# Performance work log

Hardware: AMD Instinct MI355X
Metric: run time of the kernel (lower is better)

The kernel has to match this reference:

```python
import jax, jax.numpy as jnp
import numpy as np

B, V, C, D, H, W = 1, 3, 16, 32, 256, 320


def setup_inputs() -> dict:
    key = jax.random.key(0)
    k1, k2 = jax.random.split(key)
    features = jax.random.normal(k1, (V, B, C, H, W), jnp.float32)
    # intrinsics (4x4 with 3x3 K in top-left), extrinsics with small per-view translation
    K = np.eye(4, dtype=np.float32)
    K[0, 0] = 320.0; K[1, 1] = 320.0; K[0, 2] = W / 2.0; K[1, 2] = H / 2.0
    proj = np.zeros((B, V, 2, 4, 4), np.float32)
    for v in range(V):
        E = np.eye(4, dtype=np.float32)
        E[0, 3] = 0.1 * v; E[1, 3] = 0.05 * v
        proj[:, v, 0] = E
        proj[:, v, 1] = K
    depth = jnp.linspace(425.0, 935.0, D, dtype=jnp.float32)  # DTU-style range
    depth_values = jnp.broadcast_to(depth[None, :, None, None], (B, D, H, W))
    w_reg = jax.random.normal(k2, (C,), jnp.float32) * 0.1
    return dict(features=features, proj_matrices=jnp.asarray(proj),
                depth_values=depth_values, w_reg=w_reg)


def _make_proj(pm):
    # pm: [B,2,4,4]; new[:, :3, :4] = K[:3,:3] @ E[:3,:4]
    top = jnp.einsum('bij,bjk->bik', pm[:, 1, :3, :3], pm[:, 0, :3, :4])
    return pm[:, 0].at[:, :3, :4].set(top)


def _gather_bilinear_corner(flat, xi, yi):
    # flat: [B,C,H*W]; xi, yi: int [B,D,HW] -> [B,C,D,HW] with zero padding
    valid = (xi >= 0) & (xi < W) & (yi >= 0) & (yi < H)
    idx = jnp.clip(yi, 0, H - 1) * W + jnp.clip(xi, 0, W - 1)
    b, d, n = idx.shape
    g = jnp.take_along_axis(flat, idx.reshape(b, 1, d * n), axis=2)
    g = g.reshape(b, flat.shape[1], d, n)
    return g * valid[:, None].astype(flat.dtype)


def homo_warp(src_fea, src_proj, ref_proj, depth_values):
    # src_fea [B,C,H,W], projs [B,4,4], depth_values [B,D,H,W] -> [B,C,D,H,W]
    proj = jnp.einsum('bij,bjk->bik', src_proj, jnp.linalg.inv(ref_proj))
    rot, trans = proj[:, :3, :3], proj[:, :3, 3]
    yy, xx = jnp.meshgrid(jnp.arange(H, dtype=jnp.float32),
                          jnp.arange(W, dtype=jnp.float32), indexing='ij')
    xyz = jnp.stack([xx.ravel(), yy.ravel(), jnp.ones(H * W, jnp.float32)], 0)  # [3,HW]
    rot_xyz = jnp.einsum('bij,jn->bin', rot, xyz)  # [B,3,HW]
    # [B,3,D,HW]
    pxyz = rot_xyz[:, :, None, :] * depth_values.reshape(B, 1, D, H * W) \
           + trans[:, :, None, None]
    z = pxyz[:, 2]
    z = jnp.where(jnp.abs(z) < 1e-6, 1e-6, z)
    px = pxyz[:, 0] / z  # [B,D,HW] pixel x
    py = pxyz[:, 1] / z
    x0 = jnp.floor(px); y0 = jnp.floor(py)
    wx = px - x0; wy = py - y0
    x0i = x0.astype(jnp.int32); y0i = y0.astype(jnp.int32)
    flat = src_fea.reshape(B, C, H * W)
    g00 = _gather_bilinear_corner(flat, x0i, y0i)
    g01 = _gather_bilinear_corner(flat, x0i + 1, y0i)
    g10 = _gather_bilinear_corner(flat, x0i, y0i + 1)
    g11 = _gather_bilinear_corner(flat, x0i + 1, y0i + 1)
    wx = wx[:, None]; wy = wy[:, None]
    out = (g00 * (1 - wx) * (1 - wy) + g01 * wx * (1 - wy)
           + g10 * (1 - wx) * wy + g11 * wx * wy)
    return out.reshape(B, C, D, H, W)


def _forward(features, proj_matrices, depth_values, w_reg):
    ref_fea = features[0]
    ref_proj_new = _make_proj(proj_matrices[:, 0])
    ref_vol = jnp.broadcast_to(ref_fea[:, :, None], (B, C, D, H, W))
    volume_sum = ref_vol
    volume_sq_sum = ref_vol ** 2
    for v in range(1, V):  # small fixed view loop
        src_proj_new = _make_proj(proj_matrices[:, v])
        warped = homo_warp(features[v], src_proj_new, ref_proj_new, depth_values)
        volume_sum = volume_sum + warped
        volume_sq_sum = volume_sq_sum + warped ** 2
    variance = volume_sq_sum / V - (volume_sum / V) ** 2  # [B,C,D,H,W]
    cost = jnp.einsum('bcdhw,c->bdhw', variance, w_reg)
    prob = jax.nn.softmax(cost, axis=1)  # [B,D,H,W]
    depth = jnp.sum(prob * depth_values, axis=1)  # [B,H,W]
    # confidence (no-grad branch): 2*avg_pool3d(kernel (2,1,1)) == adjacent-pair sum
    p = jax.lax.stop_gradient(prob)
    psum = p + jnp.concatenate([p[:, 1:], jnp.zeros_like(p[:, :1])], axis=1)
    didx = jnp.sum(p * jnp.arange(D, dtype=p.dtype)[None, :, None, None], axis=1)
    didx = jnp.clip(didx.astype(jnp.int32), 0, D - 1)
    conf = jnp.take_along_axis(psum, didx[:, None], axis=1)[:, 0]
    return depth, conf, prob


def reference(features, proj_matrices, depth_values, w_reg):
    return _forward(features, proj_matrices, depth_values, w_reg)
```

## Files before the change

kernel.cpp:

```cpp
#include <hip/hip_runtime.h>
#include <math.h>

namespace {
constexpr int NV = 3;
constexpr int NC = 16;
constexpr int ND = 32;
constexpr int NH = 256;
constexpr int NW = 320;
constexpr int HW = NH * NW;
#define SYM(i, j) ((i) * 4 + (j) - (i) * ((i) + 1) / 2)
}

__device__ __forceinline__ float frcp(float z) {
    float r = __builtin_amdgcn_rcpf(z);
    return r * fmaf(-z, r, 2.0f);
}

__global__ __launch_bounds__(256) void mega3_kernel(
    const float* __restrict__ feats,
    const float* __restrict__ pm,
    const float* __restrict__ dvals,
    const float* __restrict__ wreg,
    float* __restrict__ out)
{
    const unsigned tid = blockIdx.x * 256u + threadIdx.x;
    const unsigned n = tid >> 2;
    const int q = (int)(tid & 3u);
    const int d0 = q * 8;
    const int y = (int)(n / NW);
    const int x = (int)(n - (unsigned)y * NW);
    const float fx = (float)x, fy = (float)y;
    const unsigned voff = n * 4u;

    const char* fb = (const char*)feats;
    const char* f1b = fb + (size_t)1 * NC * HW * 4;
    const char* f2b = fb + (size_t)2 * NC * HW * 4;

    const float dep0 = *(const float*)((const char*)dvals + voff);
    float rf[4];
#pragma unroll
    for (int c4 = 0; c4 < 4; ++c4)
        rf[c4] = *(const float*)(fb + (size_t)(q * 4 + c4) * HW * 4 + voff);
    float dv[8];
#pragma unroll
    for (int i = 0; i < 8; ++i)
        dv[i] = *(const float*)((const char*)dvals +
                                (size_t)(d0 + i) * HW * 4 + voff);

    float P[NV][4][4];
#pragma unroll
    for (int v = 0; v < NV; ++v) {
        const float* E = pm + v * 2 * 16;
        const float* K = pm + v * 2 * 16 + 16;
#pragma unroll
        for (int j = 0; j < 4; ++j) P[v][3][j] = E[12 + j];
#pragma unroll
        for (int i = 0; i < 3; ++i)
#pragma unroll
            for (int j = 0; j < 4; ++j) {
                float acc = 0.f;
#pragma unroll
                for (int k = 0; k < 3; ++k) acc += K[i * 4 + k] * E[k * 4 + j];
                P[v][i][j] = acc;
            }
    }
    float Inv[4][4];
    {
        const float m00 = P[0][0][0], m01 = P[0][0][1], m02 = P[0][0][2], m03 = P[0][0][3];
        const float m10 = P[0][1][0], m11 = P[0][1][1], m12 = P[0][1][2], m13 = P[0][1][3];
        const float m20 = P[0][2][0], m21 = P[0][2][1], m22 = P[0][2][2], m23 = P[0][2][3];
        const float m30 = P[0][3][0], m31 = P[0][3][1], m32 = P[0][3][2], m33 = P[0][3][3];
        const float s0 = m00 * m11 - m10 * m01;
        const float s1 = m00 * m12 - m10 * m02;
        const float s2 = m00 * m13 - m10 * m03;
        const float s3 = m01 * m12 - m11 * m02;
        const float s4 = m01 * m13 - m11 * m03;
        const float s5 = m02 * m13 - m12 * m03;
        const float c5 = m22 * m33 - m32 * m23;
        const float c4_ = m21 * m33 - m31 * m23;
        const float c3 = m21 * m32 - m31 * m22;
        const float c2 = m20 * m33 - m30 * m23;
        const float c1 = m20 * m32 - m30 * m22;
        const float c0 = m20 * m31 - m30 * m21;
        const float det = s0 * c5 - s1 * c4_ + s2 * c3 + s3 * c2 - s4 * c1 + s5 * c0;
        const float id = 1.f / det;
        Inv[0][0] = ( m11 * c5 - m12 * c4_ + m13 * c3) * id;
        Inv[0][1] = (-m01 * c5 + m02 * c4_ - m03 * c3) * id;
        Inv[0][2] = ( m31 * s5 - m32 * s4 + m33 * s3) * id;
        Inv[0][3] = (-m21 * s5 + m22 * s4 - m23 * s3) * id;
        Inv[1][0] = (-m10 * c5 + m12 * c2 - m13 * c1) * id;
        Inv[1][1] = ( m00 * c5 - m02 * c2 + m03 * c1) * id;
        Inv[1][2] = (-m30 * s5 + m32 * s2 - m33 * s1) * id;
        Inv[1][3] = ( m20 * s5 - m22 * s2 + m23 * s1) * id;
        Inv[2][0] = ( m10 * c4_ - m11 * c2 + m13 * c0) * id;
        Inv[2][1] = (-m00 * c4_ + m01 * c2 - m03 * c0) * id;
        Inv[2][2] = ( m30 * s4 - m31 * s2 + m33 * s0) * id;
        Inv[2][3] = (-m20 * s4 + m21 * s2 - m23 * s0) * id;
        Inv[3][0] = (-m10 * c3 + m11 * c1 - m12 * c0) * id;
        Inv[3][1] = ( m00 * c3 - m01 * c1 + m02 * c0) * id;
        Inv[3][2] = (-m30 * s3 + m31 * s1 - m32 * s0) * id;
        Inv[3][3] = ( m20 * s3 - m21 * s1 + m22 * s0) * id;
    }
    float rxv[2], ryv[2], rzv[2], t0v[2], t1v[2], t2v[2];
#pragma unroll
    for (int v = 0; v < 2; ++v) {
        float M[3][4];
#pragma unroll
        for (int i = 0; i < 3; ++i)
#pragma unroll
            for (int j = 0; j < 4; ++j) {
                float acc = 0.f;
#pragma unroll
                for (int k = 0; k < 4; ++k) acc += P[v + 1][i][k] * Inv[k][j];
                M[i][j] = acc;
            }
        rxv[v] = fmaf(M[0][0], fx, fmaf(M[0][1], fy, M[0][2]));
        ryv[v] = fmaf(M[1][0], fx, fmaf(M[1][1], fy, M[1][2]));
        rzv[v] = fmaf(M[2][0], fx, fmaf(M[2][1], fy, M[2][2]));
        t0v[v] = M[0][3]; t1v[v] = M[1][3]; t2v[v] = M[2][3];
    }

    int x0r[2], y0r[2];
    unsigned co[2][4];
    float mk[2][4];
#pragma unroll
    for (int v = 0; v < 2; ++v) {
        float pxn = fmaf(rxv[v], dep0, t0v[v]);
        float pyn = fmaf(ryv[v], dep0, t1v[v]);
        float z   = fmaf(rzv[v], dep0, t2v[v]);
        z = (fabsf(z) < 1e-6f) ? 1e-6f : z;
        float ri = frcp(z);
        float px = pxn * ri, py = pyn * ri;
        int x0 = (int)floorf(px), y0 = (int)floorf(py);
        x0r[v] = x0; y0r[v] = y0;
        bool vx0 = (x0 >= 0) && (x0 < NW);
        bool vx1 = (x0 + 1 >= 0) && (x0 + 1 < NW);
        bool vy0 = (y0 >= 0) && (y0 < NH);
        bool vy1 = (y0 + 1 >= 0) && (y0 + 1 < NH);
        mk[v][0] = (vx0 && vy0) ? 1.f : 0.f;
        mk[v][1] = (vx1 && vy0) ? 1.f : 0.f;
        mk[v][2] = (vx0 && vy1) ? 1.f : 0.f;
        mk[v][3] = (vx1 && vy1) ? 1.f : 0.f;
        int cx0 = min(max(x0, 0), NW - 1);
        int cx1 = min(max(x0 + 1, 0), NW - 1);
        int cy0 = min(max(y0, 0), NH - 1);
        int cy1 = min(max(y0 + 1, 0), NH - 1);
        co[v][0] = (unsigned)(cy0 * NW + cx0) * 4u;
        co[v][1] = (unsigned)(cy0 * NW + cx1) * 4u;
        co[v][2] = (unsigned)(cy1 * NW + cx0) * 4u;
        co[v][3] = (unsigned)(cy1 * NW + cx1) * 4u;
    }

    float G1[10], G2[10], Cm[16], R1[4], R2[4];
    float r2 = 0.f;
#pragma unroll
    for (int k = 0; k < 10; ++k) { G1[k] = 0.f; G2[k] = 0.f; }
#pragma unroll
    for (int k = 0; k < 16; ++k) Cm[k] = 0.f;
#pragma unroll
    for (int k = 0; k < 4; ++k) { R1[k] = 0.f; R2[k] = 0.f; }

#pragma unroll
    for (int c4 = 0; c4 < 4; ++c4) {
        const int c = q * 4 + c4;
        const char* f1c = f1b + (size_t)c * HW * 4;
        const char* f2c = f2b + (size_t)c * HW * 4;
        float r = rf[c4];
        float g1[4], g2[4];
#pragma unroll
        for (int i = 0; i < 4; ++i) {
            g1[i] = *(const float*)(f1c + co[0][i]) * mk[0][i];
            g2[i] = *(const float*)(f2c + co[1][i]) * mk[1][i];
        }
        float w = wreg[c];
        float wr = w * r;
        r2 = fmaf(wr, r, r2);
        float wg1[4], wg2[4];
#pragma unroll
        for (int i = 0; i < 4; ++i) { wg1[i] = w * g1[i]; wg2[i] = w * g2[i]; }
#pragma unroll
        for (int i = 0; i < 4; ++i) {
            R1[i] = fmaf(wr, g1[i], R1[i]);
            R2[i] = fmaf(wr, g2[i], R2[i]);
        }
#pragma unroll
        for (int i = 0; i < 4; ++i)
#pragma unroll
            for (int j = i; j < 4; ++j) {
                G1[SYM(i, j)] = fmaf(wg1[i], g1[j], G1[SYM(i, j)]);
                G2[SYM(i, j)] = fmaf(wg2[i], g2[j], G2[SYM(i, j)]);
            }
#pragma unroll
        for (int i = 0; i < 4; ++i)
#pragma unroll
            for (int j = 0; j < 4; ++j)
                Cm[i * 4 + j] = fmaf(wg1[i], g2[j], Cm[i * 4 + j]);
    }

#pragma unroll
    for (int k = 0; k < 10; ++k) {
        G1[k] += __shfl_xor(G1[k], 1); G1[k] += __shfl_xor(G1[k], 2);
        G2[k] += __shfl_xor(G2[k], 1); G2[k] += __shfl_xor(G2[k], 2);
    }
#pragma unroll
    for (int k = 0; k < 16; ++k) {
        Cm[k] += __shfl_xor(Cm[k], 1); Cm[k] += __shfl_xor(Cm[k], 2);
    }
#pragma unroll
    for (int k = 0; k < 4; ++k) {
        R1[k] += __shfl_xor(R1[k], 1); R1[k] += __shfl_xor(R1[k], 2);
        R2[k] += __shfl_xor(R2[k], 1); R2[k] += __shfl_xor(R2[k], 2);
    }
    r2 += __shfl_xor(r2, 1); r2 += __shfl_xor(r2, 2);

    static constexpr float U2[3][3] = {{1.f,-2.f,1.f},{0.f,1.f,-1.f},{0.f,0.f,1.f}};
    static constexpr float U1[2][2] = {{1.f,-1.f},{0.f,1.f}};
    float A[9], Bp[9], Xc[16];
#pragma unroll
    for (int k = 0; k < 9; ++k) { A[k] = 0.f; Bp[k] = 0.f; }
#pragma unroll
    for (int k = 0; k < 16; ++k) Xc[k] = 0.f;
    A[0] = r2;
#pragma unroll
    for (int i = 0; i < 4; ++i) {
#pragma unroll
        for (int j = 0; j < 4; ++j) {
            const int lo = i < j ? i : j, hi = i < j ? j : i;
            const float g1v = G1[SYM(lo, hi)];
            const float g2v = G2[SYM(lo, hi)];
            const int m = i & 1, kk = i >> 1, nn = j & 1, ll = j >> 1;
#pragma unroll
            for (int p = 0; p < 3; ++p)
#pragma unroll
                for (int qq = 0; qq < 3; ++qq) {
                    const float cc = U2[m + nn][p] * U2[kk + ll][qq];
                    if (cc != 0.f) {
                        A[p * 3 + qq] += g1v * cc;
                        Bp[p * 3 + qq] += g2v * cc;
                    }
                }
        }
    }
#pragma unroll
    for (int i = 0; i < 4; ++i) {
        const int m = i & 1, kk = i >> 1;
#pragma unroll
        for (int p = 0; p < 2; ++p)
#pragma unroll
            for (int qq = 0; qq < 2; ++qq) {
                const float cc = U1[m][p] * U1[kk][qq];
                if (cc != 0.f) {
                    A[p * 3 + qq] -= R1[i] * cc;
                    Bp[p * 3 + qq] -= R2[i] * cc;
                }
            }
    }
#pragma unroll
    for (int i = 0; i < 4; ++i) {
        const int m = i & 1, kk = i >> 1;
#pragma unroll
        for (int j = 0; j < 4; ++j) {
            const int nn = j & 1, ll = j >> 1;
            const float cv = Cm[i * 4 + j];
#pragma unroll
            for (int p = 0; p < 2; ++p)
#pragma unroll
                for (int qq = 0; qq < 2; ++qq)
#pragma unroll
                    for (int rr = 0; rr < 2; ++rr)
#pragma unroll
                        for (int ss = 0; ss < 2; ++ss) {
                            const float cc = U1[m][p] * U1[kk][qq]
                                           * U1[nn][rr] * U1[ll][ss];
                            if (cc != 0.f)
                                Xc[p * 8 + qq * 4 + rr * 2 + ss] -= cv * cc;
                        }
        }
    }

    float c[8];
    float mx = -INFINITY;
#pragma unroll
    for (int ck = 0; ck < 2; ++ck) {
        float pxs[2][4], pys[2][4];
#pragma unroll
        for (int dd = 0; dd < 4; ++dd) {
            const float depth = dv[ck * 4 + dd];
#pragma unroll
            for (int v = 0; v < 2; ++v) {
                float pxn = fmaf(rxv[v], depth, t0v[v]);
                float pyn = fmaf(ryv[v], depth, t1v[v]);
                float z   = fmaf(rzv[v], depth, t2v[v]);
                z = (fabsf(z) < 1e-6f) ? 1e-6f : z;
                float ri = frcp(z);
                pxs[v][dd] = pxn * ri;
                pys[v][dd] = pyn * ri;
            }
        }
#pragma unroll
        for (int dd = 0; dd < 4; ++dd) {
            float wx[2], wy[2];
            int ax0[2], ay0[2];
            bool fast = true;
#pragma unroll
            for (int v = 0; v < 2; ++v) {
                float px = pxs[v][dd], py = pys[v][dd];
                float x0f = floorf(px), y0f = floorf(py);
                wx[v] = px - x0f;
                wy[v] = py - y0f;
                int x0 = (int)x0f, y0 = (int)y0f;
                ax0[v] = x0; ay0[v] = y0;
                fast = fast && (x0 == x0r[v]) && (y0 == y0r[v]);
            }

            float cst;
            if (fast) {
                const float wx0 = wx[0], wy0 = wy[0];
                const float wx1 = wx[1], wy1 = wy[1];
                float a0 = fmaf(wy0, fmaf(wy0, A[2], A[1]), A[0]);
                float a1 = fmaf(wy0, fmaf(wy0, A[5], A[4]), A[3]);
                float a2 = fmaf(wy0, fmaf(wy0, A[8], A[7]), A[6]);
                float PA = fmaf(wx0, fmaf(wx0, a2, a1), a0);
                float b0 = fmaf(wy1, fmaf(wy1, Bp[2], Bp[1]), Bp[0]);
                float b1 = fmaf(wy1, fmaf(wy1, Bp[5], Bp[4]), Bp[3]);
                float b2 = fmaf(wy1, fmaf(wy1, Bp[8], Bp[7]), Bp[6]);
                float PB = fmaf(wx1, fmaf(wx1, b2, b1), b0);
                float y0_ = fmaf(wy1, Xc[1], Xc[0]);
                float y1_ = fmaf(wy1, Xc[3], Xc[2]);
                float y2_ = fmaf(wy1, Xc[5], Xc[4]);
                float y3_ = fmaf(wy1, Xc[7], Xc[6]);
                float y4_ = fmaf(wy1, Xc[9], Xc[8]);
                float y5_ = fmaf(wy1, Xc[11], Xc[10]);
                float y6_ = fmaf(wy1, Xc[13], Xc[12]);
                float y7_ = fmaf(wy1, Xc[15], Xc[14]);
                float z0_ = fmaf(wx1, y1_, y0_);
                float z1_ = fmaf(wx1, y3_, y2_);
                float z2_ = fmaf(wx1, y5_, y4_);
                float z3_ = fmaf(wx1, y7_, y6_);
                float w0_ = fmaf(wy0, z1_, z0_);
                float w1_ = fmaf(wy0, z3_, z2_);
                float Xv = fmaf(wx0, w1_, w0_);
                cst = (2.f / 9.f) * (PA + PB + Xv);
            } else {
                float al[2][4];
                unsigned so[2][4];
#pragma unroll
                for (int v = 0; v < 2; ++v) {
                    int x0 = ax0[v], y0 = ay0[v];
                    bool vx0 = (x0 >= 0) && (x0 < NW);
                    bool vx1 = (x0 + 1 >= 0) && (x0 + 1 < NW);
                    bool vy0 = (y0 >= 0) && (y0 < NH);
                    bool vy1 = (y0 + 1 >= 0) && (y0 + 1 < NH);
                    float wxx = wx[v], wyy = wy[v];
                    al[v][0] = (1.f - wxx) * (1.f - wyy) * ((vx0 && vy0) ? 1.f : 0.f);
                    al[v][1] = wxx * (1.f - wyy) * ((vx1 && vy0) ? 1.f : 0.f);
                    al[v][2] = (1.f - wxx) * wyy * ((vx0 && vy1) ? 1.f : 0.f);
                    al[v][3] = wxx * wyy * ((vx1 && vy1) ? 1.f : 0.f);
                    int cx0 = min(max(x0, 0), NW - 1);
                    int cx1 = min(max(x0 + 1, 0), NW - 1);
                    int cy0 = min(max(y0, 0), NH - 1);
                    int cy1 = min(max(y0 + 1, 0), NH - 1);
                    so[v][0] = (unsigned)(cy0 * NW + cx0) * 4u;
                    so[v][1] = (unsigned)(cy0 * NW + cx1) * 4u;
                    so[v][2] = (unsigned)(cy1 * NW + cx0) * 4u;
                    so[v][3] = (unsigned)(cy1 * NW + cx1) * 4u;
                }
                float acc = 0.f;
#pragma unroll
                for (int cc = 0; cc < NC; ++cc) {
                    const char* frc = fb + (size_t)cc * HW * 4;
                    const char* f1c = f1b + (size_t)cc * HW * 4;
                    const char* f2c = f2b + (size_t)cc * HW * 4;
                    float r = *(const float*)(frc + voff);
                    float s1 = 0.f, s2 = 0.f;
#pragma unroll
                    for (int i = 0; i < 4; ++i) {
                        s1 = fmaf(*(const float*)(f1c + so[0][i]), al[0][i], s1);
                        s2 = fmaf(*(const float*)(f2c + so[1][i]), al[1][i], s2);
                    }
                    float e = r * r + s1 * s1 + s2 * s2
                            - r * s1 - r * s2 - s1 * s2;
                    acc = fmaf(wreg[cc], e, acc);
                }
                cst = (2.f / 9.f) * acc;
            }
            c[ck * 4 + dd] = cst;
            mx = fmaxf(mx, cst);
        }
    }

    mx = fmaxf(mx, __shfl_xor(mx, 1));
    mx = fmaxf(mx, __shfl_xor(mx, 2));
    float ssum = 0.f;
#pragma unroll
    for (int i = 0; i < 8; ++i) {
        float e = __expf(c[i] - mx);
        c[i] = e;
        ssum += e;
    }
    ssum += __shfl_xor(ssum, 1);
    ssum += __shfl_xor(ssum, 2);
    float inv = 1.f / ssum;

    float* prob = out + 2 * HW;
    float depth_acc = 0.f, didx_acc = 0.f;
#pragma unroll
    for (int i = 0; i < 8; ++i) {
        float pv = c[i] * inv;
        c[i] = pv;
        *(float*)((char*)prob + (size_t)(d0 + i) * HW * 4 + voff) = pv;
        depth_acc = fmaf(pv, dv[i], depth_acc);
        didx_acc = fmaf(pv, (float)(d0 + i), didx_acc);
    }
    depth_acc += __shfl_xor(depth_acc, 1);
    depth_acc += __shfl_xor(depth_acc, 2);
    didx_acc += __shfl_xor(didx_acc, 1);
    didx_acc += __shfl_xor(didx_acc, 2);

    int di = (int)didx_acc;
    di = min(max(di, 0), ND - 1);
    float pdi = 0.f, pdi1 = 0.f;
#pragma unroll
    for (int i = 0; i < 8; ++i) {
        pdi  = (d0 + i == di)     ? c[i] : pdi;
        pdi1 = (d0 + i == di + 1) ? c[i] : pdi1;
    }
    pdi  += __shfl_xor(pdi, 1);
    pdi  += __shfl_xor(pdi, 2);
    pdi1 += __shfl_xor(pdi1, 1);
    pdi1 += __shfl_xor(pdi1, 2);

    if (q == 0) {
        out[n] = depth_acc;
        out[HW + n] = pdi + pdi1;
    }
}

extern "C" void kernel_launch(void* const* d_in, const int* in_sizes, int n_in,
                              void* d_out, int out_size, void* d_ws, size_t ws_size,
                              hipStream_t stream) {
    const float* feats = (const float*)d_in[0];
    const float* pm    = (const float*)d_in[1];
    const float* dvals = (const float*)d_in[2];
    const float* wreg  = (const float*)d_in[3];
    float* out = (float*)d_out;
    (void)d_ws; (void)ws_size;

    mega3_kernel<<<HW * 4 / 256, 256, 0, stream>>>(feats, pm, dvals, wreg,
                                                   out);
}
```

Before: 26.43 us.

## Split each pixel across eight lanes and evaluate cost via direct bilinear quadratic form

Each pixel is now handled by eight lanes instead of four, so each lane covers two channels and four depths, and the launch grid doubles. The polynomial-basis precomputation (A, Bp, Xc) is dropped. The fast path instead evaluates the variance cost directly as a quadratic form over the bilinear weights, using the Gram, cross and linear terms, with off-diagonal Gram entries doubled. This is meant to raise parallelism and cut per-thread register pressure and setup work. In exchange it adds an extra shuffle stage to every reduction and more per-depth arithmetic in the fast path.

```diff
diff --git a/kernel.cpp b/kernel.cpp
--- a/kernel.cpp
+++ b/kernel.cpp
@@ -16,7 +16,7 @@
     return r * fmaf(-z, r, 2.0f);
 }
 
-__global__ __launch_bounds__(256) void mega3_kernel(
+__global__ __launch_bounds__(256) void mega4_kernel(
     const float* __restrict__ feats,
     const float* __restrict__ pm,
     const float* __restrict__ dvals,
@@ -24,9 +24,9 @@
     float* __restrict__ out)
 {
     const unsigned tid = blockIdx.x * 256u + threadIdx.x;
-    const unsigned n = tid >> 2;
-    const int q = (int)(tid & 3u);
-    const int d0 = q * 8;
+    const unsigned n = tid >> 3;
+    const int r8 = (int)(tid & 7u);
+    const int d0 = r8 * 4;
     const int y = (int)(n / NW);
     const int x = (int)(n - (unsigned)y * NW);
     const float fx = (float)x, fy = (float)y;
@@ -37,13 +37,13 @@
     const char* f2b = fb + (size_t)2 * NC * HW * 4;
 
     const float dep0 = *(const float*)((const char*)dvals + voff);
-    float rf[4];
-#pragma unroll
-    for (int c4 = 0; c4 < 4; ++c4)
-        rf[c4] = *(const float*)(fb + (size_t)(q * 4 + c4) * HW * 4 + voff);
-    float dv[8];
-#pragma unroll
-    for (int i = 0; i < 8; ++i)
+    float rf[2];
+#pragma unroll
+    for (int c2 = 0; c2 < 2; ++c2)
+        rf[c2] = *(const float*)(fb + (size_t)(r8 * 2 + c2) * HW * 4 + voff);
+    float dv[4];
+#pragma unroll
+    for (int i = 0; i < 4; ++i)
         dv[i] = *(const float*)((const char*)dvals +
                                 (size_t)(d0 + i) * HW * 4 + voff);
 
@@ -161,11 +161,11 @@
     for (int k = 0; k < 4; ++k) { R1[k] = 0.f; R2[k] = 0.f; }
 
 #pragma unroll
-    for (int c4 = 0; c4 < 4; ++c4) {
-        const int c = q * 4 + c4;
+    for (int c2 = 0; c2 < 2; ++c2) {
+        const int c = r8 * 2 + c2;
         const char* f1c = f1b + (size_t)c * HW * 4;
         const char* f2c = f2b + (size_t)c * HW * 4;
-        float r = rf[c4];
+        float r = rf[c2];
         float g1[4], g2[4];
 #pragma unroll
         for (int i = 0; i < 4; ++i) {
@@ -200,92 +200,39 @@
 #pragma unroll
     for (int k = 0; k < 10; ++k) {
         G1[k] += __shfl_xor(G1[k], 1); G1[k] += __shfl_xor(G1[k], 2);
+        G1[k] += __shfl_xor(G1[k], 4);
         G2[k] += __shfl_xor(G2[k], 1); G2[k] += __shfl_xor(G2[k], 2);
+        G2[k] += __shfl_xor(G2[k], 4);
     }
 #pragma unroll
     for (int k = 0; k < 16; ++k) {
         Cm[k] += __shfl_xor(Cm[k], 1); Cm[k] += __shfl_xor(Cm[k], 2);
+        Cm[k] += __shfl_xor(Cm[k], 4);
     }
 #pragma unroll
     for (int k = 0; k < 4; ++k) {
         R1[k] += __shfl_xor(R1[k], 1); R1[k] += __shfl_xor(R1[k], 2);
+        R1[k] += __shfl_xor(R1[k], 4);
         R2[k] += __shfl_xor(R2[k], 1); R2[k] += __shfl_xor(R2[k], 2);
-    }
-    r2 += __shfl_xor(r2, 1); r2 += __shfl_xor(r2, 2);
-
-    static constexpr float U2[3][3] = {{1.f,-2.f,1.f},{0.f,1.f,-1.f},{0.f,0.f,1.f}};
-    static constexpr float U1[2][2] = {{1.f,-1.f},{0.f,1.f}};
-    float A[9], Bp[9], Xc[16];
-#pragma unroll
-    for (int k = 0; k < 9; ++k) { A[k] = 0.f; Bp[k] = 0.f; }
-#pragma unroll
-    for (int k = 0; k < 16; ++k) Xc[k] = 0.f;
-    A[0] = r2;
-#pragma unroll
-    for (int i = 0; i < 4; ++i) {
-#pragma unroll
-        for (int j = 0; j < 4; ++j) {
-            const int lo = i < j ? i : j, hi = i < j ? j : i;
-            const float g1v = G1[SYM(lo, hi)];
-            const float g2v = G2[SYM(lo, hi)];
-            const int m = i & 1, kk = i >> 1, nn = j & 1, ll = j >> 1;
-#pragma unroll
-            for (int p = 0; p < 3; ++p)
-#pragma unroll
-                for (int qq = 0; qq < 3; ++qq) {
-                    const float cc = U2[m + nn][p] * U2[kk + ll][qq];
-                    if (cc != 0.f) {
-                        A[p * 3 + qq] += g1v * cc;
-                        Bp[p * 3 + qq] += g2v * cc;
-                    }
-                }
+        R2[k] += __shfl_xor(R2[k], 4);
+    }
+    r2 += __shfl_xor(r2, 1); r2 += __shfl_xor(r2, 2); r2 += __shfl_xor(r2, 4);
+
+#pragma unroll
+    for (int i = 0; i < 4; ++i)
+#pragma unroll
+        for (int j = i + 1; j < 4; ++j) {
+            G1[SYM(i, j)] += G1[SYM(i, j)];
+            G2[SYM(i, j)] += G2[SYM(i, j)];
         }
-    }
-#pragma unroll
-    for (int i = 0; i < 4; ++i) {
-        const int m = i & 1, kk = i >> 1;
-#pragma unroll
-        for (int p = 0; p < 2; ++p)
-#pragma unroll
-            for (int qq = 0; qq < 2; ++qq) {
-                const float cc = U1[m][p] * U1[kk][qq];
-                if (cc != 0.f) {
-                    A[p * 3 + qq] -= R1[i] * cc;
-                    Bp[p * 3 + qq] -= R2[i] * cc;
-                }
-            }
-    }
-#pragma unroll
-    for (int i = 0; i < 4; ++i) {
-        const int m = i & 1, kk = i >> 1;
-#pragma unroll
-        for (int j = 0; j < 4; ++j) {
-            const int nn = j & 1, ll = j >> 1;
-            const float cv = Cm[i * 4 + j];
-#pragma unroll
-            for (int p = 0; p < 2; ++p)
-#pragma unroll
-                for (int qq = 0; qq < 2; ++qq)
-#pragma unroll
-                    for (int rr = 0; rr < 2; ++rr)
-#pragma unroll
-                        for (int ss = 0; ss < 2; ++ss) {
-                            const float cc = U1[m][p] * U1[kk][qq]
-                                           * U1[nn][rr] * U1[ll][ss];
-                            if (cc != 0.f)
-                                Xc[p * 8 + qq * 4 + rr * 2 + ss] -= cv * cc;
-                        }
-        }
-    }
-
-    float c[8];
+
+    float c[4];
     float mx = -INFINITY;
-#pragma unroll
-    for (int ck = 0; ck < 2; ++ck) {
+    {
         float pxs[2][4], pys[2][4];
 #pragma unroll
         for (int dd = 0; dd < 4; ++dd) {
-            const float depth = dv[ck * 4 + dd];
+            const float depth = dv[dd];
 #pragma unroll
             for (int v = 0; v < 2; ++v) {
                 float pxn = fmaf(rxv[v], depth, t0v[v]);
@@ -315,32 +262,40 @@
 
             float cst;
             if (fast) {
-                const float wx0 = wx[0], wy0 = wy[0];
-                const float wx1 = wx[1], wy1 = wy[1];
-                float a0 = fmaf(wy0, fmaf(wy0, A[2], A[1]), A[0]);
-                float a1 = fmaf(wy0, fmaf(wy0, A[5], A[4]), A[3]);
-                float a2 = fmaf(wy0, fmaf(wy0, A[8], A[7]), A[6]);
-                float PA = fmaf(wx0, fmaf(wx0, a2, a1), a0);
-                float b0 = fmaf(wy1, fmaf(wy1, Bp[2], Bp[1]), Bp[0]);
-                float b1 = fmaf(wy1, fmaf(wy1, Bp[5], Bp[4]), Bp[3]);
-                float b2 = fmaf(wy1, fmaf(wy1, Bp[8], Bp[7]), Bp[6]);
-                float PB = fmaf(wx1, fmaf(wx1, b2, b1), b0);
-                float y0_ = fmaf(wy1, Xc[1], Xc[0]);
-                float y1_ = fmaf(wy1, Xc[3], Xc[2]);
-                float y2_ = fmaf(wy1, Xc[5], Xc[4]);
-                float y3_ = fmaf(wy1, Xc[7], Xc[6]);
-                float y4_ = fmaf(wy1, Xc[9], Xc[8]);
-                float y5_ = fmaf(wy1, Xc[11], Xc[10]);
-                float y6_ = fmaf(wy1, Xc[13], Xc[12]);
-                float y7_ = fmaf(wy1, Xc[15], Xc[14]);
-                float z0_ = fmaf(wx1, y1_, y0_);
-                float z1_ = fmaf(wx1, y3_, y2_);
-                float z2_ = fmaf(wx1, y5_, y4_);
-                float z3_ = fmaf(wx1, y7_, y6_);
-                float w0_ = fmaf(wy0, z1_, z0_);
-                float w1_ = fmaf(wy0, z3_, z2_);
-                float Xv = fmaf(wx0, w1_, w0_);
-                cst = (2.f / 9.f) * (PA + PB + Xv);
+                float al0[4], al1[4];
+                {
+                    float wxx = wx[0], wyy = wy[0];
+                    al0[0] = (1.f - wxx) * (1.f - wyy);
+                    al0[1] = wxx * (1.f - wyy);
+                    al0[2] = (1.f - wxx) * wyy;
+                    al0[3] = wxx * wyy;
+                    wxx = wx[1]; wyy = wy[1];
+                    al1[0] = (1.f - wxx) * (1.f - wyy);
+                    al1[1] = wxx * (1.f - wyy);
+                    al1[2] = (1.f - wxx) * wyy;
+                    al1[3] = wxx * wyy;
+                }
+                float q1 = 0.f, q2 = 0.f;
+#pragma unroll
+                for (int i = 0; i < 4; ++i)
+#pragma unroll
+                    for (int j = i; j < 4; ++j) {
+                        q1 = fmaf(G1[SYM(i, j)], al0[i] * al0[j], q1);
+                        q2 = fmaf(G2[SYM(i, j)], al1[i] * al1[j], q2);
+                    }
+                float qc = 0.f;
+#pragma unroll
+                for (int i = 0; i < 4; ++i)
+#pragma unroll
+                    for (int j = 0; j < 4; ++j)
+                        qc = fmaf(Cm[i * 4 + j], al0[i] * al1[j], qc);
+                float lr = 0.f;
+#pragma unroll
+                for (int i = 0; i < 4; ++i) {
+                    lr = fmaf(R1[i], al0[i], lr);
+                    lr = fmaf(R2[i], al1[i], lr);
+                }
+                cst = (2.f / 9.f) * (r2 + q1 + q2 - lr - qc);
             } else {
                 float al[2][4];
                 unsigned so[2][4];
@@ -384,28 +339,30 @@
                 }
                 cst = (2.f / 9.f) * acc;
             }
-            c[ck * 4 + dd] = cst;
+            c[dd] = cst;
             mx = fmaxf(mx, cst);
         }
     }
 
     mx = fmaxf(mx, __shfl_xor(mx, 1));
     mx = fmaxf(mx, __shfl_xor(mx, 2));
+    mx = fmaxf(mx, __shfl_xor(mx, 4));
     float ssum = 0.f;
 #pragma unroll
-    for (int i = 0; i < 8; ++i) {
+    for (int i = 0; i < 4; ++i) {
         float e = __expf(c[i] - mx);
         c[i] = e;
         ssum += e;
     }
     ssum += __shfl_xor(ssum, 1);
     ssum += __shfl_xor(ssum, 2);
+    ssum += __shfl_xor(ssum, 4);
     float inv = 1.f / ssum;
 
     float* prob = out + 2 * HW;
     float depth_acc = 0.f, didx_acc = 0.f;
 #pragma unroll
-    for (int i = 0; i < 8; ++i) {
+    for (int i = 0; i < 4; ++i) {
         float pv = c[i] * inv;
         c[i] = pv;
         *(float*)((char*)prob + (size_t)(d0 + i) * HW * 4 + voff) = pv;
@@ -414,23 +371,27 @@
     }
     depth_acc += __shfl_xor(depth_acc, 1);
     depth_acc += __shfl_xor(depth_acc, 2);
+    depth_acc += __shfl_xor(depth_acc, 4);
     didx_acc += __shfl_xor(didx_acc, 1);
     didx_acc += __shfl_xor(didx_acc, 2);
+    didx_acc += __shfl_xor(didx_acc, 4);
 
     int di = (int)didx_acc;
     di = min(max(di, 0), ND - 1);
     float pdi = 0.f, pdi1 = 0.f;
 #pragma unroll
-    for (int i = 0; i < 8; ++i) {
+    for (int i = 0; i < 4; ++i) {
         pdi  = (d0 + i == di)     ? c[i] : pdi;
         pdi1 = (d0 + i == di + 1) ? c[i] : pdi1;
     }
     pdi  += __shfl_xor(pdi, 1);
     pdi  += __shfl_xor(pdi, 2);
+    pdi  += __shfl_xor(pdi, 4);
     pdi1 += __shfl_xor(pdi1, 1);
     pdi1 += __shfl_xor(pdi1, 2);
-
-    if (q == 0) {
+    pdi1 += __shfl_xor(pdi1, 4);
+
+    if (r8 == 0) {
         out[n] = depth_acc;
         out[HW + n] = pdi + pdi1;
     }
@@ -446,6 +407,6 @@
     float* out = (float*)d_out;
     (void)d_ws; (void)ws_size;
 
-    mega3_kernel<<<HW * 4 / 256, 256, 0, stream>>>(feats, pm, dvals, wreg,
+    mega4_kernel<<<HW * 8 / 256, 256, 0, stream>>>(feats, pm, dvals, wreg,
                                                    out);
 }
```

Measured after the change: 40.77 us. 54.3% more time.
